# Optimization experiments

Hardware: AMD Instinct MI355X
Metric: run time of the kernel (lower is better)

Reference implementation:

```python
import jax, jax.numpy as jnp
import numpy as np

N, E = 50000, 800000
IN_FEATS, HID, HEADS = 128, 32, 4
NEG_SLOPE = 0.2


def gat_layer(x, W, al, ar, b, src, dst):
    # x: [N, F_in], W: [F_in, H*D], al/ar: [H, D], b: [H*D]
    h = (x @ W).reshape(N, HEADS, HID)          # [N, H, D]
    el = jnp.einsum('nhd,hd->nh', h, al)        # [N, H]
    er = jnp.einsum('nhd,hd->nh', h, ar)        # [N, H]
    e = el[src] + er[dst]                       # [E, H]
    e = jnp.where(e > 0, e, NEG_SLOPE * e)      # LeakyReLU(0.2)
    # edge softmax over incoming edges of each dst node (numerically stable)
    m = jax.ops.segment_max(e, dst, num_segments=N)      # [N, H]
    m = jnp.where(jnp.isfinite(m), m, 0.0)
    a = jnp.exp(e - m[dst])                     # [E, H]
    denom = jax.ops.segment_sum(a, dst, num_segments=N)  # [N, H]
    alpha = a / jnp.maximum(denom[dst], 1e-9)   # [E, H]
    msg = alpha[:, :, None] * h[src]            # [E, H, D]
    out = jax.ops.segment_sum(msg, dst, num_segments=N)  # [N, H, D]
    out = out + b.reshape(1, HEADS, HID)
    return out.reshape(N, HEADS * HID)


def setup_inputs() -> dict:
    key = jax.random.key(0)
    ks = jax.random.split(key, 12)
    def glorot(k, shape):
        fan = sum(shape)
        return jax.random.normal(k, shape, jnp.float32) * jnp.sqrt(2.0 / fan)
    return {
        'features': jax.random.normal(ks[0], (N, IN_FEATS), jnp.float32),
        'src': jax.random.randint(ks[1], (E,), 0, N, jnp.int32),
        'dst': jax.random.randint(ks[2], (E,), 0, N, jnp.int32),
        'W1': glorot(ks[3], (IN_FEATS, HEADS * HID)),
        'al1': glorot(ks[4], (HEADS, HID)),
        'ar1': glorot(ks[5], (HEADS, HID)),
        'b1': jnp.zeros((HEADS * HID,), jnp.float32),
        'W2': glorot(ks[6], (HEADS * HID, HEADS * HID)),
        'al2': glorot(ks[7], (HEADS, HID)),
        'ar2': glorot(ks[8], (HEADS, HID)),
        'b2': jnp.zeros((HEADS * HID,), jnp.float32),
    }


def reference(features, src, dst, W1, al1, ar1, b1, W2, al2, ar2, b2):
    # dropout(p=0.6) is identity at inference (training=False)
    x = gat_layer(features, W1, al1, ar1, b1, src, dst)
    x = jax.nn.elu(x)
    x = gat_layer(x, W2, al2, ar2, b2, src, dst)
    x = jax.nn.elu(x)
    return x  # [N, HEADS*HID]
```

## Files before the change

kernel.cpp:

```cpp
#include <hip/hip_runtime.h>

#define F 128
#define HEADS 4
#define HID 32
#define LS 136
#define SLOTS 64
#define CS 16

typedef __attribute__((ext_vector_type(8))) short short8;
typedef __attribute__((ext_vector_type(4))) float f32x4;

static __device__ __forceinline__ unsigned short f2bf(float f) {
  unsigned u = __float_as_uint(f);
  unsigned r = (u + 0x7fffu + ((u >> 16) & 1u)) >> 16;
  return (unsigned short)r;
}
static __device__ __forceinline__ float bf2f(unsigned short h) {
  return __uint_as_float(((unsigned)h) << 16);
}

__global__ __launch_bounds__(256) void prep_k(const float* __restrict__ W1,
                                              const float* __restrict__ W2,
                                              unsigned short* __restrict__ WT1,
                                              unsigned short* __restrict__ WT2,
                                              int* __restrict__ cnt, int N) {
  int b = blockIdx.x;
  if (b < 128) {
    int gid = b * 256 + threadIdx.x;
    int wsel = gid >> 14;
    int idx = gid & 16383;
    int n = idx >> 7, k = idx & 127;
    const float* W = wsel ? W2 : W1;
    unsigned short* WT = wsel ? WT2 : WT1;
    WT[n * 128 + k] = f2bf(W[k * 128 + n]);
  } else {
    int zid = (b - 128) * 256 + threadIdx.x;
    int total = N * CS;
    int total4 = total >> 2;
    int4* c4 = (int4*)cnt;
    for (int i = zid; i < total4; i += 128 * 256) c4[i] = make_int4(0, 0, 0, 0);
    if (zid < (total & 3)) cnt[(total4 << 2) + zid] = 0;
  }
}

__global__ __launch_bounds__(256) void scatter_k(const int* __restrict__ src,
                                                 const int* __restrict__ dst,
                                                 int* __restrict__ cnt,
                                                 int* __restrict__ csr_src,
                                                 int E, int N, int CE4) {
  int grp = blockIdx.x & 7;
  int blk = blockIdx.x >> 3;
  int RN = (N + 7) >> 3;
  int lo = grp * RN;
  int hi = lo + RN; if (hi > N) hi = N;
  int E4 = E >> 2;
  int e0 = blk * CE4;
  int e1 = e0 + CE4; if (e1 > E4) e1 = E4;
  const int4* dst4 = (const int4*)dst;
  for (int e = e0 + (int)threadIdx.x; e < e1; e += 256) {
    int4 d4 = dst4[e];
    int eb = 4 * e;
#pragma unroll
    for (int k = 0; k < 4; ++k) {
      int d = (k == 0) ? d4.x : (k == 1) ? d4.y : (k == 2) ? d4.z : d4.w;
      if (d >= lo && d < hi) {
        int pos = atomicAdd(&cnt[(size_t)d * CS], 1);
        if (pos < SLOTS)
          csr_src[(size_t)d * SLOTS + pos] = __builtin_nontemporal_load(&src[eb + k]);
      }
    }
  }
  if (blk == 0) {
    for (int e = (E4 << 2) + (int)threadIdx.x; e < E; e += 256) {
      int d = dst[e];
      if (d >= lo && d < hi) {
        int pos = atomicAdd(&cnt[(size_t)d * CS], 1);
        if (pos < SLOTS)
          csr_src[(size_t)d * SLOTS + pos] = __builtin_nontemporal_load(&src[e]);
      }
    }
  }
}

__global__ __launch_bounds__(256) void gemm_mfma_k(const float* __restrict__ Xf,
                                                   const unsigned short* __restrict__ Xb,
                                                   const unsigned short* __restrict__ WT,
                                                   const float* __restrict__ alf,
                                                   const float* __restrict__ arf,
                                                   unsigned short* __restrict__ hb,
                                                   float* __restrict__ el,
                                                   float* __restrict__ er, int N) {
  __shared__ unsigned short wt_s[128 * LS];
  __shared__ unsigned short xs[64 * LS];
  int tid = threadIdx.x;
  int n0 = blockIdx.x * 64;

#pragma unroll
  for (int j = 0; j < 8; ++j) {
    int c = tid + 256 * j;
    int n = c >> 4, seg = c & 15;
    *(uint4*)&wt_s[n * LS + seg * 8] = *(const uint4*)&WT[n * 128 + seg * 8];
  }
  if (Xb) {
#pragma unroll
    for (int j = 0; j < 4; ++j) {
      int c = tid + 256 * j;
      int r = c >> 4, seg = c & 15;
      uint4 v = make_uint4(0u, 0u, 0u, 0u);
      if (n0 + r < N) v = *(const uint4*)&Xb[(long)(n0 + r) * F + seg * 8];
      *(uint4*)&xs[r * LS + seg * 8] = v;
    }
  } else {
#pragma unroll
    for (int j = 0; j < 8; ++j) {
      int c = tid + 256 * j;
      int r = c >> 5, c4 = c & 31;
      float4 v = make_float4(0.f, 0.f, 0.f, 0.f);
      if (n0 + r < N) v = *(const float4*)&Xf[(long)(n0 + r) * F + c4 * 4];
      unsigned lo = (unsigned)f2bf(v.x) | ((unsigned)f2bf(v.y) << 16);
      unsigned hi = (unsigned)f2bf(v.z) | ((unsigned)f2bf(v.w) << 16);
      *(uint2*)&xs[r * LS + c4 * 4] = make_uint2(lo, hi);
    }
  }
  __syncthreads();

  int w = tid >> 6, lane = tid & 63;
  int l15 = lane & 15, quad = lane >> 4;
  f32x4 acc[8];
#pragma unroll
  for (int nt = 0; nt < 8; ++nt) acc[nt] = (f32x4){0.f, 0.f, 0.f, 0.f};

  const unsigned short* arow = &xs[(16 * w + l15) * LS + quad * 8];
#pragma unroll
  for (int kk = 0; kk < 4; ++kk) {
    short8 a = *(const short8*)(arow + kk * 32);
#pragma unroll
    for (int nt = 0; nt < 8; ++nt) {
      short8 b = *(const short8*)&wt_s[(nt * 16 + l15) * LS + kk * 32 + quad * 8];
      acc[nt] = __builtin_amdgcn_mfma_f32_16x16x32_bf16(a, b, acc[nt], 0, 0, 0);
    }
  }

  __syncthreads();
#pragma unroll
  for (int nt = 0; nt < 8; ++nt)
#pragma unroll
    for (int r = 0; r < 4; ++r)
      xs[(16 * w + quad * 4 + r) * LS + nt * 16 + l15] = f2bf(acc[nt][r]);
  __syncthreads();

#pragma unroll
  for (int j = 0; j < 4; ++j) {
    int c = tid + 256 * j;
    int r = c >> 4, seg = c & 15;
    if (n0 + r < N)
      *(uint4*)&hb[(long)(n0 + r) * F + seg * 8] = *(uint4*)&xs[r * LS + seg * 8];
  }
  {
    int r = tid >> 2, hd = tid & 3;
    const unsigned short* base = &xs[r * LS + hd * HID];
    float sl = 0.f, sr = 0.f;
#pragma unroll
    for (int d = 0; d < HID; ++d) {
      float hv = bf2f(base[d]);
      sl += hv * alf[hd * HID + d];
      sr += hv * arf[hd * HID + d];
    }
    if (n0 + r < N) { el[(n0 + r) * 4 + hd] = sl; er[(n0 + r) * 4 + hd] = sr; }
  }
}

__global__ __launch_bounds__(256) void agg_k(const int* __restrict__ cnt,
                                             const int* __restrict__ csr_src,
                                             const float* __restrict__ el,
                                             const float* __restrict__ er,
                                             const unsigned short* __restrict__ hb,
                                             const float* __restrict__ bias,
                                             float* __restrict__ out,
                                             unsigned short* __restrict__ outb, int N) {
  int d = (blockIdx.x * blockDim.x + threadIdx.x) >> 6;
  int lane = threadIdx.x & 63;
  if (d >= N) return;
  int q = lane & 31;
  int p = lane >> 5;
  int hdw = lane >> 4;
  int hd16 = (q >> 3) * 16;
  int svr = csr_src[(size_t)d * SLOTS + lane];
  int cn = cnt[(size_t)d * CS];
  float erd = er[d * 4 + hdw];
  if (cn > SLOTS) cn = SLOTS;
  int sv = (lane < cn) ? svr : 0;

  float acc0 = 0.f, acc1 = 0.f, acc2 = 0.f, acc3 = 0.f, asum = 0.f;
#pragma unroll 4
  for (int sub = 0; sub < 4; ++sub) {
    int sb = sub * 16;
    if (sb >= cn) break;

    uint2 hv[8];
#pragma unroll
    for (int jj = 0; jj < 4; ++jj) {
      int j = 4 * jj;
      int sA = __shfl(sv, sb + j + p);
      int sB = __shfl(sv, sb + j + 2 + p);
      hv[2 * jj]     = *(const uint2*)(hb + (unsigned)sA * 128u + (unsigned)q * 4u);
      hv[2 * jj + 1] = *(const uint2*)(hb + (unsigned)sB * 128u + (unsigned)q * 4u);
    }

    int idx = sb + (lane & 15);
    int se = __shfl(sv, idx);
    float e = el[(unsigned)se * 4u + hdw] + erd;
    e = e > 0.f ? e : 0.2f * e;
    float wgt = __expf(e);
    if (idx >= cn) wgt = 0.f;
    float wv[8];
#pragma unroll
    for (int jj = 0; jj < 4; ++jj) {
      int j = 4 * jj;
      wv[2 * jj]     = __shfl(wgt, hd16 + j + p);
      wv[2 * jj + 1] = __shfl(wgt, hd16 + j + 2 + p);
    }

#pragma unroll
    for (int jj = 0; jj < 8; ++jj) {
      float w = wv[jj];
      uint2 hh = hv[jj];
      acc0 += w * __uint_as_float(hh.x << 16);
      acc1 += w * __uint_as_float(hh.x & 0xffff0000u);
      acc2 += w * __uint_as_float(hh.y << 16);
      acc3 += w * __uint_as_float(hh.y & 0xffff0000u);
      asum += w;
    }
  }
  asum += __shfl_xor(asum, 32);
  acc0 += __shfl_xor(acc0, 32);
  acc1 += __shfl_xor(acc1, 32);
  acc2 += __shfl_xor(acc2, 32);
  acc3 += __shfl_xor(acc3, 32);
  float inv = 1.f / fmaxf(asum, 1e-9f);
  float4 bv = *(const float4*)&bias[4 * q];
  float o0 = acc0 * inv + bv.x;
  float o1 = acc1 * inv + bv.y;
  float o2 = acc2 * inv + bv.z;
  float o3 = acc3 * inv + bv.w;
  o0 = o0 > 0.f ? o0 : (__expf(o0) - 1.f);
  o1 = o1 > 0.f ? o1 : (__expf(o1) - 1.f);
  o2 = o2 > 0.f ? o2 : (__expf(o2) - 1.f);
  o3 = o3 > 0.f ? o3 : (__expf(o3) - 1.f);
  if (p == 0) {
    if (outb) {
      unsigned lo = (unsigned)f2bf(o0) | ((unsigned)f2bf(o1) << 16);
      unsigned hi = (unsigned)f2bf(o2) | ((unsigned)f2bf(o3) << 16);
      *(uint2*)&outb[(size_t)d * F + 4 * q] = make_uint2(lo, hi);
    } else {
      *(float4*)&out[(size_t)d * F + 4 * q] = make_float4(o0, o1, o2, o3);
    }
  }
}

extern "C" void kernel_launch(void* const* d_in, const int* in_sizes, int n_in,
                              void* d_out, int out_size, void* d_ws, size_t ws_size,
                              hipStream_t stream) {
  const float* feat = (const float*)d_in[0];
  const int*   src  = (const int*)d_in[1];
  const int*   dst  = (const int*)d_in[2];
  const float* W1   = (const float*)d_in[3];
  const float* al1  = (const float*)d_in[4];
  const float* ar1  = (const float*)d_in[5];
  const float* b1   = (const float*)d_in[6];
  const float* W2   = (const float*)d_in[7];
  const float* al2  = (const float*)d_in[8];
  const float* ar2  = (const float*)d_in[9];
  const float* b2   = (const float*)d_in[10];
  float* out = (float*)d_out;
  int N = in_sizes[0] / F;
  int E = in_sizes[1];

  char* ws = (char*)d_ws;
  auto align256 = [](size_t x) { return (x + 255) & ~(size_t)255; };
  int* cnt     = (int*)ws; ws += align256((size_t)N * CS * 4);
  int* csr_src = (int*)ws; ws += align256((size_t)N * SLOTS * 4);
  float* el    = (float*)ws; ws += align256((size_t)N * HEADS * 4);
  float* er    = (float*)ws; ws += align256((size_t)N * HEADS * 4);
  unsigned short* hb  = (unsigned short*)ws; ws += align256((size_t)N * F * 2);
  unsigned short* xb  = (unsigned short*)ws; ws += align256((size_t)N * F * 2);
  unsigned short* WT1 = (unsigned short*)ws; ws += align256((size_t)F * F * 2);
  unsigned short* WT2 = (unsigned short*)ws; ws += align256((size_t)F * F * 2);

  prep_k<<<256, 256, 0, stream>>>(W1, W2, WT1, WT2, cnt, N);

  {
    int G = 256;
    int E4 = E >> 2;
    int CE4 = (E4 + G - 1) / G;
    scatter_k<<<8 * G, 256, 0, stream>>>(src, dst, cnt, csr_src, E, N, CE4);
  }

  int gemmBlocks = (N + 63) / 64;
  int aggBlocks  = (N + 3) / 4;

  gemm_mfma_k<<<gemmBlocks, 256, 0, stream>>>(feat, nullptr, WT1, al1, ar1, hb, el, er, N);
  agg_k<<<aggBlocks, 256, 0, stream>>>(cnt, csr_src, el, er, hb, b1, out, xb, N);

  gemm_mfma_k<<<gemmBlocks, 256, 0, stream>>>(nullptr, xb, WT2, al2, ar2, hb, el, er, N);
  agg_k<<<aggBlocks, 256, 0, stream>>>(cnt, csr_src, el, er, hb, b2, out, nullptr, N);
}
```

Baseline: 236.4 us.

## Fuse layer-1 GEMM and edge scatter into one heterogeneous launch

Merges the CSR scatter kernel and the first-layer GEMM into one kernel. One in four blocks runs the GEMM and the rest run scatter work, so the compute-bound MFMA GEMM overlaps the atomic-heavy scatter and one launch boundary goes away. The cost is that every scatter block now reserves the GEMM's shared memory, which can lower occupancy for the scatter part. The block interleaving also adds some tail imbalance.

```diff
diff --git a/kernel.cpp b/kernel.cpp
--- a/kernel.cpp
+++ b/kernel.cpp
@@ -6,6 +6,7 @@
 #define LS 136
 #define SLOTS 64
 #define CS 16
+#define SBLK 2048
 
 typedef __attribute__((ext_vector_type(8))) short short8;
 typedef __attribute__((ext_vector_type(4))) float f32x4;
@@ -43,13 +44,11 @@
   }
 }
 
-__global__ __launch_bounds__(256) void scatter_k(const int* __restrict__ src,
-                                                 const int* __restrict__ dst,
-                                                 int* __restrict__ cnt,
-                                                 int* __restrict__ csr_src,
-                                                 int E, int N, int CE4) {
-  int grp = blockIdx.x & 7;
-  int blk = blockIdx.x >> 3;
+static __device__ __forceinline__ void scatter_body(int sb, int tid,
+    const int* __restrict__ src, const int* __restrict__ dst,
+    int* __restrict__ cnt, int* __restrict__ csr_src, int E, int N, int CE4) {
+  int grp = sb & 7;
+  int blk = sb >> 3;
   int RN = (N + 7) >> 3;
   int lo = grp * RN;
   int hi = lo + RN; if (hi > N) hi = N;
@@ -57,7 +56,7 @@
   int e0 = blk * CE4;
   int e1 = e0 + CE4; if (e1 > E4) e1 = E4;
   const int4* dst4 = (const int4*)dst;
-  for (int e = e0 + (int)threadIdx.x; e < e1; e += 256) {
+  for (int e = e0 + tid; e < e1; e += 256) {
     int4 d4 = dst4[e];
     int eb = 4 * e;
 #pragma unroll
@@ -71,7 +70,7 @@
     }
   }
   if (blk == 0) {
-    for (int e = (E4 << 2) + (int)threadIdx.x; e < E; e += 256) {
+    for (int e = (E4 << 2) + tid; e < E; e += 256) {
       int d = dst[e];
       if (d >= lo && d < hi) {
         int pos = atomicAdd(&cnt[(size_t)d * CS], 1);
@@ -82,8 +81,114 @@
   }
 }
 
-__global__ __launch_bounds__(256) void gemm_mfma_k(const float* __restrict__ Xf,
-                                                   const unsigned short* __restrict__ Xb,
+static __device__ __forceinline__ void gemm_body(int bid, int tid,
+    const float* __restrict__ Xf, const unsigned short* __restrict__ Xb,
+    const unsigned short* __restrict__ WT,
+    const float* __restrict__ alf, const float* __restrict__ arf,
+    unsigned short* __restrict__ hb, float* __restrict__ el,
+    float* __restrict__ er, int N,
+    unsigned short* wt_s, unsigned short* xs) {
+  int n0 = bid * 64;
+
+#pragma unroll
+  for (int j = 0; j < 8; ++j) {
+    int c = tid + 256 * j;
+    int n = c >> 4, seg = c & 15;
+    *(uint4*)&wt_s[n * LS + seg * 8] = *(const uint4*)&WT[n * 128 + seg * 8];
+  }
+  if (Xb) {
+#pragma unroll
+    for (int j = 0; j < 4; ++j) {
+      int c = tid + 256 * j;
+      int r = c >> 4, seg = c & 15;
+      uint4 v = make_uint4(0u, 0u, 0u, 0u);
+      if (n0 + r < N) v = *(const uint4*)&Xb[(long)(n0 + r) * F + seg * 8];
+      *(uint4*)&xs[r * LS + seg * 8] = v;
+    }
+  } else {
+#pragma unroll
+    for (int j = 0; j < 8; ++j) {
+      int c = tid + 256 * j;
+      int r = c >> 5, c4 = c & 31;
+      float4 v = make_float4(0.f, 0.f, 0.f, 0.f);
+      if (n0 + r < N) v = *(const float4*)&Xf[(long)(n0 + r) * F + c4 * 4];
+      unsigned lo = (unsigned)f2bf(v.x) | ((unsigned)f2bf(v.y) << 16);
+      unsigned hi = (unsigned)f2bf(v.z) | ((unsigned)f2bf(v.w) << 16);
+      *(uint2*)&xs[r * LS + c4 * 4] = make_uint2(lo, hi);
+    }
+  }
+  __syncthreads();
+
+  int w = tid >> 6, lane = tid & 63;
+  int l15 = lane & 15, quad = lane >> 4;
+  f32x4 acc[8];
+#pragma unroll
+  for (int nt = 0; nt < 8; ++nt) acc[nt] = (f32x4){0.f, 0.f, 0.f, 0.f};
+
+  const unsigned short* arow = &xs[(16 * w + l15) * LS + quad * 8];
+#pragma unroll
+  for (int kk = 0; kk < 4; ++kk) {
+    short8 a = *(const short8*)(arow + kk * 32);
+#pragma unroll
+    for (int nt = 0; nt < 8; ++nt) {
+      short8 b = *(const short8*)&wt_s[(nt * 16 + l15) * LS + kk * 32 + quad * 8];
+      acc[nt] = __builtin_amdgcn_mfma_f32_16x16x32_bf16(a, b, acc[nt], 0, 0, 0);
+    }
+  }
+
+  __syncthreads();
+#pragma unroll
+  for (int nt = 0; nt < 8; ++nt)
+#pragma unroll
+    for (int r = 0; r < 4; ++r)
+      xs[(16 * w + quad * 4 + r) * LS + nt * 16 + l15] = f2bf(acc[nt][r]);
+  __syncthreads();
+
+#pragma unroll
+  for (int j = 0; j < 4; ++j) {
+    int c = tid + 256 * j;
+    int r = c >> 4, seg = c & 15;
+    if (n0 + r < N)
+      *(uint4*)&hb[(long)(n0 + r) * F + seg * 8] = *(uint4*)&xs[r * LS + seg * 8];
+  }
+  {
+    int r = tid >> 2, hd = tid & 3;
+    const unsigned short* base = &xs[r * LS + hd * HID];
+    float sl = 0.f, sr = 0.f;
+#pragma unroll
+    for (int d = 0; d < HID; ++d) {
+      float hv = bf2f(base[d]);
+      sl += hv * alf[hd * HID + d];
+      sr += hv * arf[hd * HID + d];
+    }
+    if (n0 + r < N) { el[(n0 + r) * 4 + hd] = sl; er[(n0 + r) * 4 + hd] = sr; }
+  }
+}
+
+__global__ __launch_bounds__(256) void fused_gs_k(
+    const float* __restrict__ Xf, const unsigned short* __restrict__ WT,
+    const float* __restrict__ alf, const float* __restrict__ arf,
+    unsigned short* __restrict__ hb, float* __restrict__ el,
+    float* __restrict__ er,
+    const int* __restrict__ src, const int* __restrict__ dst,
+    int* __restrict__ cnt, int* __restrict__ csr_src,
+    int E, int N, int CE4, int gemmBlocks) {
+  __shared__ unsigned short wt_s[128 * LS];
+  __shared__ unsigned short xs[64 * LS];
+  int b = blockIdx.x;
+  int tid = threadIdx.x;
+  if ((b & 3) == 0) {
+    int gb = b >> 2;
+    if (gb < gemmBlocks)
+      gemm_body(gb, tid, Xf, nullptr, WT, alf, arf, hb, el, er, N, wt_s, xs);
+  } else {
+    int sb = b - (b >> 2) - 1;
+    if (sb < SBLK)
+      scatter_body(sb, tid, src, dst, cnt, csr_src, E, N, CE4);
+  }
+}
+
+__global__ __launch_bounds__(256) void gemm_mfma_k(const unsigned short* __restrict__ Xb,
                                                    const unsigned short* __restrict__ WT,
                                                    const float* __restrict__ alf,
                                                    const float* __restrict__ arf,
@@ -92,82 +197,7 @@
                                                    float* __restrict__ er, int N) {
   __shared__ unsigned short wt_s[128 * LS];
   __shared__ unsigned short xs[64 * LS];
-  int tid = threadIdx.x;
-  int n0 = blockIdx.x * 64;
-
-#pragma unroll
-  for (int j = 0; j < 8; ++j) {
-    int c = tid + 256 * j;
-    int n = c >> 4, seg = c & 15;
-    *(uint4*)&wt_s[n * LS + seg * 8] = *(const uint4*)&WT[n * 128 + seg * 8];
-  }
-  if (Xb) {
-#pragma unroll
-    for (int j = 0; j < 4; ++j) {
-      int c = tid + 256 * j;
-      int r = c >> 4, seg = c & 15;
-      uint4 v = make_uint4(0u, 0u, 0u, 0u);
-      if (n0 + r < N) v = *(const uint4*)&Xb[(long)(n0 + r) * F + seg * 8];
-      *(uint4*)&xs[r * LS + seg * 8] = v;
-    }
-  } else {
-#pragma unroll
-    for (int j = 0; j < 8; ++j) {
-      int c = tid + 256 * j;
-      int r = c >> 5, c4 = c & 31;
-      float4 v = make_float4(0.f, 0.f, 0.f, 0.f);
-      if (n0 + r < N) v = *(const float4*)&Xf[(long)(n0 + r) * F + c4 * 4];
-      unsigned lo = (unsigned)f2bf(v.x) | ((unsigned)f2bf(v.y) << 16);
-      unsigned hi = (unsigned)f2bf(v.z) | ((unsigned)f2bf(v.w) << 16);
-      *(uint2*)&xs[r * LS + c4 * 4] = make_uint2(lo, hi);
-    }
-  }
-  __syncthreads();
-
-  int w = tid >> 6, lane = tid & 63;
-  int l15 = lane & 15, quad = lane >> 4;
-  f32x4 acc[8];
-#pragma unroll
-  for (int nt = 0; nt < 8; ++nt) acc[nt] = (f32x4){0.f, 0.f, 0.f, 0.f};
-
-  const unsigned short* arow = &xs[(16 * w + l15) * LS + quad * 8];
-#pragma unroll
-  for (int kk = 0; kk < 4; ++kk) {
-    short8 a = *(const short8*)(arow + kk * 32);
-#pragma unroll
-    for (int nt = 0; nt < 8; ++nt) {
-      short8 b = *(const short8*)&wt_s[(nt * 16 + l15) * LS + kk * 32 + quad * 8];
-      acc[nt] = __builtin_amdgcn_mfma_f32_16x16x32_bf16(a, b, acc[nt], 0, 0, 0);
-    }
-  }
-
-  __syncthreads();
-#pragma unroll
-  for (int nt = 0; nt < 8; ++nt)
-#pragma unroll
-    for (int r = 0; r < 4; ++r)
-      xs[(16 * w + quad * 4 + r) * LS + nt * 16 + l15] = f2bf(acc[nt][r]);
-  __syncthreads();
-
-#pragma unroll
-  for (int j = 0; j < 4; ++j) {
-    int c = tid + 256 * j;
-    int r = c >> 4, seg = c & 15;
-    if (n0 + r < N)
-      *(uint4*)&hb[(long)(n0 + r) * F + seg * 8] = *(uint4*)&xs[r * LS + seg * 8];
-  }
-  {
-    int r = tid >> 2, hd = tid & 3;
-    const unsigned short* base = &xs[r * LS + hd * HID];
-    float sl = 0.f, sr = 0.f;
-#pragma unroll
-    for (int d = 0; d < HID; ++d) {
-      float hv = bf2f(base[d]);
-      sl += hv * alf[hd * HID + d];
-      sr += hv * arf[hd * HID + d];
-    }
-    if (n0 + r < N) { el[(n0 + r) * 4 + hd] = sl; er[(n0 + r) * 4 + hd] = sr; }
-  }
+  gemm_body(blockIdx.x, threadIdx.x, nullptr, Xb, WT, alf, arf, hb, el, er, N, wt_s, xs);
 }
 
 __global__ __launch_bounds__(256) void agg_k(const int* __restrict__ cnt,
@@ -287,21 +317,23 @@
   unsigned short* WT1 = (unsigned short*)ws; ws += align256((size_t)F * F * 2);
   unsigned short* WT2 = (unsigned short*)ws; ws += align256((size_t)F * F * 2);
 
-  prep_k<<<256, 256, 0, stream>>>(W1, W2, WT1, WT2, cnt, N);
-
-  {
-    int G = 256;
-    int E4 = E >> 2;
-    int CE4 = (E4 + G - 1) / G;
-    scatter_k<<<8 * G, 256, 0, stream>>>(src, dst, cnt, csr_src, E, N, CE4);
-  }
-
   int gemmBlocks = (N + 63) / 64;
   int aggBlocks  = (N + 3) / 4;
 
-  gemm_mfma_k<<<gemmBlocks, 256, 0, stream>>>(feat, nullptr, WT1, al1, ar1, hb, el, er, N);
+  int fg = 4 * gemmBlocks;
+  while (fg - (fg + 3) / 4 < SBLK) fg += 4;
+
+  int G = 256;
+  int E4 = E >> 2;
+  int CE4 = (E4 + G - 1) / G;
+
+  prep_k<<<256, 256, 0, stream>>>(W1, W2, WT1, WT2, cnt, N);
+
+  fused_gs_k<<<fg, 256, 0, stream>>>(feat, WT1, al1, ar1, hb, el, er,
+                                     src, dst, cnt, csr_src, E, N, CE4, gemmBlocks);
+
   agg_k<<<aggBlocks, 256, 0, stream>>>(cnt, csr_src, el, er, hb, b1, out, xb, N);
 
-  gemm_mfma_k<<<gemmBlocks, 256, 0, stream>>>(nullptr, xb, WT2, al2, ar2, hb, el, er, N);
+  gemm_mfma_k<<<gemmBlocks, 256, 0, stream>>>(xb, WT2, al2, ar2, hb, el, er, N);
   agg_k<<<aggBlocks, 256, 0, stream>>>(cnt, csr_src, el, er, hb, b2, out, nullptr, N);
 }
```

Measured after the change: 263.8 us. 11.6% more time.
